# Kernel tuning notes

Measured on AMD Instinct MI355X. Metric: run time of the kernel, lower is better.

The kernel has to match this reference:

```python
import jax, jax.numpy as jnp
import numpy as np

D_MODEL = 1024
N_HEADS = 16
D_K = D_MODEL // N_HEADS
ROPE_BASE = 500000.0
RMS_EPS = 1e-10


def _rms_norm(x, w):
    # RMSNorm over last dim (per-head d_k): w * x / sqrt(mean(x^2) + eps)
    rms = jnp.sqrt(jnp.mean(x * x, axis=-1, keepdims=True) + RMS_EPS)
    return w * (x / rms)


def _rotate_half(x):
    x1, x2 = x[..., : x.shape[-1] // 2], x[..., x.shape[-1] // 2:]
    return jnp.concatenate([-x2, x1], axis=-1)


def _rope_cos_sin(seq_len):
    inv_freq = 1.0 / (ROPE_BASE ** (jnp.arange(0, D_K, 2, dtype=jnp.float32) / D_K))
    t = jnp.arange(seq_len, dtype=jnp.float32)
    freqs = jnp.outer(t, inv_freq)                # (S, d_k/2)
    emb = jnp.concatenate([freqs, freqs], axis=-1)  # (S, d_k)
    return jnp.cos(emb), jnp.sin(emb)


def setup_inputs() -> dict:
    key = jax.random.key(0)
    ks = jax.random.split(key, 9)
    B, S, D = 2, 2048, D_MODEL
    scale = 1.0 / np.sqrt(D)
    return {
        "q": jax.random.normal(ks[0], (B, S, D), jnp.float32),
        "k": jax.random.normal(ks[1], (B, S, D), jnp.float32),
        "v": jax.random.normal(ks[2], (B, S, D), jnp.float32),
        "w_q": jax.random.normal(ks[3], (D, D), jnp.float32) * scale,
        "w_k": jax.random.normal(ks[4], (D, D), jnp.float32) * scale,
        "w_v": jax.random.normal(ks[5], (D, D), jnp.float32) * scale,
        "w_o": jax.random.normal(ks[6], (D, D), jnp.float32) * scale,
        "q_norm_w": jnp.ones((D_K,), jnp.float32),
        "k_norm_w": jnp.ones((D_K,), jnp.float32),
    }


def reference(q, k, v, w_q, w_k, w_v, w_o, q_norm_w, k_norm_w):
    B, S, D = q.shape
    H, Dk = N_HEADS, D_K

    # QKV projections (nn.Linear without bias: x @ W.T), split into heads
    query = jnp.einsum("bsd,ed->bse", q, w_q).reshape(B, S, H, Dk).transpose(0, 2, 1, 3)
    key_ = jnp.einsum("bsd,ed->bse", k, w_k).reshape(B, S, H, Dk).transpose(0, 2, 1, 3)
    value = jnp.einsum("bsd,ed->bse", v, w_v).reshape(B, S, H, Dk).transpose(0, 2, 1, 3)

    # QK-norm (per-head RMSNorm)
    query = _rms_norm(query, q_norm_w)
    key_ = _rms_norm(key_, k_norm_w)

    # RoPE, default positions 0..S-1
    cos, sin = _rope_cos_sin(S)          # (S, d_k)
    cos = cos[None, None]                # (1,1,S,d_k)
    sin = sin[None, None]
    query = query * cos + _rotate_half(query) * sin
    key_ = key_ * cos + _rotate_half(key_) * sin

    # Causal scaled dot-product attention
    scale = 1.0 / jnp.sqrt(jnp.asarray(Dk, query.dtype))
    scores = jnp.einsum("bhqd,bhkd->bhqk", query, key_) * scale
    causal = jnp.tril(jnp.ones((S, S), dtype=bool))
    scores = jnp.where(causal, scores, jnp.finfo(scores.dtype).min)
    attn = jax.nn.softmax(scores, axis=-1)
    out = jnp.einsum("bhqk,bhkd->bhqd", attn, value)  # (B,H,S,d_k)

    out = out.transpose(0, 2, 1, 3).reshape(B, S, D)
    return jnp.einsum("bsd,ed->bse", out, w_o)
```

## Files before the change

### kernel.cpp

```cpp
#include <hip/hip_runtime.h>
#include <cstdint>
#include <cstddef>

typedef __bf16 bf16;
typedef __bf16 bf16x4_t __attribute__((ext_vector_type(4)));
typedef __bf16 bf16x8_t __attribute__((ext_vector_type(8)));
typedef float  f32x4_t  __attribute__((ext_vector_type(4)));

#define GLD_LDS16(g, l)                                                              \
  __builtin_amdgcn_global_load_lds((const __attribute__((address_space(1))) void*)(g), \
                                   (__attribute__((address_space(3))) void*)(l), 16, 0, 0)

#define S_WAITCNT_VMCNT(N) asm volatile("s_waitcnt vmcnt(" #N ")" ::: "memory")
#define S_BARRIER() asm volatile("s_barrier" ::: "memory")

__global__ __launch_bounds__(256) void cvt_kernel(
    const float* __restrict__ q, const float* __restrict__ k, const float* __restrict__ v,
    const float* __restrict__ wq, const float* __restrict__ wk, const float* __restrict__ wv,
    const float* __restrict__ wo,
    bf16* __restrict__ qb, bf16* __restrict__ kb, bf16* __restrict__ vb,
    bf16* __restrict__ wqb, bf16* __restrict__ wkb, bf16* __restrict__ wvb,
    bf16* __restrict__ wob)
{
  const float* src; bf16* dst; int n;
  switch (blockIdx.y) {
    case 0: src = q;  dst = qb;  n = 4194304; break;
    case 1: src = k;  dst = kb;  n = 4194304; break;
    case 2: src = v;  dst = vb;  n = 4194304; break;
    case 3: src = wq; dst = wqb; n = 1048576; break;
    case 4: src = wk; dst = wkb; n = 1048576; break;
    case 5: src = wv; dst = wvb; n = 1048576; break;
    default: src = wo; dst = wob; n = 1048576; break;
  }
  const int i = (blockIdx.x * 256 + threadIdx.x) * 4;
  if (i >= n) return;
  const float4 f = *(const float4*)(src + i);
  bf16x4_t o;
  o[0] = (bf16)f.x; o[1] = (bf16)f.y; o[2] = (bf16)f.z; o[3] = (bf16)f.w;
  *(bf16x4_t*)(dst + i) = o;
}

__device__ __forceinline__ void gemm_core(const bf16* __restrict__ A,
                                          const bf16* __restrict__ W,
                                          int m0, int n0, f32x4_t (&acc)[4][4])
{
  const int K = 1024;
  __shared__ bf16 As[3][128 * 32];
  __shared__ bf16 Bs[3][128 * 32];
  const int t = threadIdx.x;
  const int lane = t & 63, w = t >> 6;
  const int l16 = lane & 15, qd = lane >> 4;
  const int wm = (w & 1) * 64, wn = (w >> 1) * 64;

  const int srow = t >> 2;
  const int skey = (srow & 3) ^ ((srow >> 2) & 3);
  const int scol = ((t & 3) ^ skey) * 8;
  const bf16* ag0 = A + (size_t)(m0 + srow) * K + scol;
  const bf16* ag1 = A + (size_t)(m0 + 64 + srow) * K + scol;
  const bf16* wg0 = W + (size_t)(n0 + srow) * K + scol;
  const bf16* wg1 = W + (size_t)(n0 + 64 + srow) * K + scol;
  const int lo0 = (w * 64) * 8;
  const int lo1 = (256 + w * 64) * 8;

  const int sw = (l16 & 3) ^ ((l16 >> 2) & 3);

#define STAGEG(k0_, b_)                         \
  do {                                          \
    GLD_LDS16(ag0 + (k0_), &As[b_][lo0]);       \
    GLD_LDS16(ag1 + (k0_), &As[b_][lo1]);       \
    GLD_LDS16(wg0 + (k0_), &Bs[b_][lo0]);       \
    GLD_LDS16(wg1 + (k0_), &Bs[b_][lo1]);       \
  } while (0)

  STAGEG(0, 0);
  STAGEG(32, 1);

  for (int k0 = 0; k0 < K; k0 += 32) {
    const int it = k0 >> 5;
    const int cb = it - (it / 3) * 3;
    if (k0 + 32 < K) S_WAITCNT_VMCNT(4); else S_WAITCNT_VMCNT(0);
    S_BARRIER();
    if (k0 + 64 < K) {
      const int nb = (it + 2) - ((it + 2) / 3) * 3;
      STAGEG(k0 + 64, nb);
    }
    bf16x8_t af[4], bfg[4];
#pragma unroll
    for (int i = 0; i < 4; ++i)
      af[i] = *(const bf16x8_t*)(&As[cb][(wm + i * 16 + l16) * 32 + (qd ^ sw) * 8]);
#pragma unroll
    for (int j = 0; j < 4; ++j)
      bfg[j] = *(const bf16x8_t*)(&Bs[cb][(wn + j * 16 + l16) * 32 + (qd ^ sw) * 8]);
#pragma unroll
    for (int i = 0; i < 4; ++i)
#pragma unroll
      for (int j = 0; j < 4; ++j)
        acc[i][j] = __builtin_amdgcn_mfma_f32_16x16x32_bf16(af[i], bfg[j], acc[i][j], 0, 0, 0);
  }
#undef STAGEG
}

__global__ __launch_bounds__(256) void gemm_qkv(
    const bf16* __restrict__ qb, const bf16* __restrict__ wqb,
    const bf16* __restrict__ kb, const bf16* __restrict__ wkb,
    const bf16* __restrict__ vb, const bf16* __restrict__ wvb,
    const float* __restrict__ qnw, const float* __restrict__ knw,
    bf16* __restrict__ Qp, bf16* __restrict__ Kp, bf16* __restrict__ Vt)
{
  const int z = blockIdx.z;
  const bf16 *A, *W;
  if (z == 0)      { A = qb; W = wqb; }
  else if (z == 1) { A = kb; W = wkb; }
  else             { A = vb; W = wvb; }

  const int m0 = blockIdx.y * 128, n0 = blockIdx.x * 128;
  f32x4_t acc[4][4] = {};
  gemm_core(A, W, m0, n0, acc);

  const int t = threadIdx.x;
  const int lane = t & 63, w = t >> 6;
  const int l16 = lane & 15, qd = lane >> 4;
  const int wm = (w & 1) * 64;
  const int h = blockIdx.x * 2 + (w >> 1);
  const int b = m0 >> 11;

  if (z == 2) {
#pragma unroll
    for (int i = 0; i < 4; ++i) {
      const int sq = (m0 & 2047) + wm + i * 16 + qd * 4;
      const int pos = (sq & ~31) + 8 * qd + 4 * (i & 1);
#pragma unroll
      for (int j = 0; j < 4; ++j) {
        const int dk = j * 16 + l16;
        bf16x4_t ov;
#pragma unroll
        for (int r = 0; r < 4; ++r) ov[r] = (bf16)acc[i][j][r];
        *(bf16x4_t*)(Vt + ((size_t)((b * 16 + h) * 64 + dk)) * 2048 + pos) = ov;
      }
    }
    return;
  }

  const float* nw = (z == 0) ? qnw : knw;
  const float osc = (z == 0) ? 0.125f * 1.44269504088896f : 1.0f;
  bf16* Out = (z == 0) ? Qp : Kp;

  float nwv[4];
#pragma unroll
  for (int j = 0; j < 4; ++j) nwv[j] = nw[j * 16 + l16];
  float invf[2];
#pragma unroll
  for (int jj = 0; jj < 2; ++jj) {
    const int d = jj * 16 + l16;
    invf[jj] = __builtin_amdgcn_exp2f(-(float)(2 * d) * (18.93156857f / 64.0f)) * 0.15915494309f;
  }

#pragma unroll
  for (int i = 0; i < 4; ++i) {
    const int sbase = (m0 & 2047) + wm + i * 16 + qd * 4;
    float ssq[4];
#pragma unroll
    for (int r = 0; r < 4; ++r) {
      ssq[r] = 0.f;
#pragma unroll
      for (int j = 0; j < 4; ++j) ssq[r] += acc[i][j][r] * acc[i][j][r];
    }
#pragma unroll
    for (int off = 1; off < 16; off <<= 1)
#pragma unroll
      for (int r = 0; r < 4; ++r) ssq[r] += __shfl_xor(ssq[r], off);

    float xn[4][4];
#pragma unroll
    for (int r = 0; r < 4; ++r) {
      const float inv = 1.0f / sqrtf(ssq[r] * (1.0f / 64.0f) + 1e-10f);
#pragma unroll
      for (int j = 0; j < 4; ++j) xn[j][r] = acc[i][j][r] * inv * nwv[j];
    }
#pragma unroll
    for (int jj = 0; jj < 2; ++jj) {
      const int d = jj * 16 + l16;
#pragma unroll
      for (int r = 0; r < 4; ++r) {
        const int s = sbase + r;
        float rev = (float)s * invf[jj];
        rev = rev - floorf(rev);
        const float cv = __builtin_amdgcn_cosf(rev);
        const float sv = __builtin_amdgcn_sinf(rev);
        const float o1 = (xn[jj][r] * cv - xn[jj + 2][r] * sv) * osc;
        const float o2 = (xn[jj + 2][r] * cv + xn[jj][r] * sv) * osc;
        bf16* base = Out + ((size_t)(b * 16 + h) * 2048 + s) * 64;
        base[d] = (bf16)o1;
        base[d + 32] = (bf16)o2;
      }
    }
  }
}

__global__ __launch_bounds__(256) void gemm_out_k(
    const bf16* __restrict__ Ob, const bf16* __restrict__ wob, float* __restrict__ out)
{
  const int N = 1024;
  const int m0 = blockIdx.y * 128, n0 = blockIdx.x * 128;
  f32x4_t acc[4][4] = {};
  gemm_core(Ob, wob, m0, n0, acc);

  const int t = threadIdx.x;
  const int lane = t & 63, w = t >> 6;
  const int l16 = lane & 15, qd = lane >> 4;
  const int wm = (w & 1) * 64, wn = (w >> 1) * 64;
#pragma unroll
  for (int i = 0; i < 4; ++i) {
    const int row = m0 + wm + i * 16 + qd * 4;
#pragma unroll
    for (int j = 0; j < 4; ++j) {
      const int col = n0 + wn + j * 16 + l16;
#pragma unroll
      for (int r = 0; r < 4; ++r)
        out[(size_t)(row + r) * N + col] = acc[i][j][r];
    }
  }
}

__global__ __launch_bounds__(512) void flash_attn(
    const bf16* __restrict__ Qp, const bf16* __restrict__ Kp,
    const bf16* __restrict__ Vt, bf16* __restrict__ O)
{
  const int S = 2048;
  const int qt = 15 - blockIdx.x;
  const int bh = blockIdx.y;
  const int t = threadIdx.x;
  const int lane = t & 63, w = t >> 6;
  const int l16 = lane & 15, qd = lane >> 4;

  __shared__ bf16 Ks[3][64 * 64];
  __shared__ bf16 Vs[3][64 * 64];

  const int qrow = qt * 128 + w * 16 + l16;
  const bf16* qbase = Qp + ((size_t)bh * S + qrow) * 64 + qd * 8;
  const bf16x8_t qf0 = *(const bf16x8_t*)qbase;
  const bf16x8_t qf1 = *(const bf16x8_t*)(qbase + 32);

  f32x4_t o_acc[4] = {};
  float l_i = 0.f;

  const int srow = t >> 3;
  const int scol = ((t & 7) ^ (srow & 7)) * 8;
  const bf16* kg = Kp + ((size_t)bh * S + srow) * 64 + scol;
  const bf16* vg = Vt + ((size_t)(bh * 64 + srow)) * S + scol;
  const int lo = w * 512;

  const int sw = l16 & 7;

#define STAGE(kt_, b_)                                 \
  do {                                                 \
    GLD_LDS16(kg + (size_t)(kt_) * 4096, &Ks[b_][lo]); \
    GLD_LDS16(vg + (kt_) * 64, &Vs[b_][lo]);           \
  } while (0)

  const int ktmax = 2 * qt + 1;
  STAGE(0, 0);
  STAGE(1, 1);

  for (int kt = 0; kt <= ktmax; ++kt) {
    const int cb = kt - (kt / 3) * 3;
    if (kt < ktmax) S_WAITCNT_VMCNT(2); else S_WAITCNT_VMCNT(0);
    S_BARRIER();
    if (kt + 2 <= ktmax) {
      const int nb = (kt + 2) - ((kt + 2) / 3) * 3;
      STAGE(kt + 2, nb);
    }

    if (kt == ktmax && w < 4) continue;

    f32x4_t sf[4];
#pragma unroll
    for (int nt = 0; nt < 4; ++nt) {
      sf[nt][0] = -12.f; sf[nt][1] = -12.f; sf[nt][2] = -12.f; sf[nt][3] = -12.f;
      const bf16x8_t kf0 = *(const bf16x8_t*)(&Ks[cb][(nt * 16 + l16) * 64 + ((0 + qd) ^ sw) * 8]);
      const bf16x8_t kf1 = *(const bf16x8_t*)(&Ks[cb][(nt * 16 + l16) * 64 + ((4 + qd) ^ sw) * 8]);
      sf[nt] = __builtin_amdgcn_mfma_f32_16x16x32_bf16(kf0, qf0, sf[nt], 0, 0, 0);
      sf[nt] = __builtin_amdgcn_mfma_f32_16x16x32_bf16(kf1, qf1, sf[nt], 0, 0, 0);
    }

    if (kt >= ktmax - 1) {
      const int kofs = (kt - 2 * qt) * 64;
      const int q_local = w * 16 + l16;
#pragma unroll
      for (int nt = 0; nt < 4; ++nt)
#pragma unroll
        for (int r = 0; r < 4; ++r)
          if (kofs + nt * 16 + qd * 4 + r > q_local) sf[nt][r] = -100.f;
    }

    bf16x4_t pb[4];
#pragma unroll
    for (int nt = 0; nt < 4; ++nt)
#pragma unroll
      for (int r = 0; r < 4; ++r) {
        const float p = __builtin_amdgcn_exp2f(sf[nt][r]);
        l_i += p;
        pb[nt][r] = (bf16)p;
      }

#pragma unroll
    for (int nt2 = 0; nt2 < 2; ++nt2) {
      bf16x8_t pf;
#pragma unroll
      for (int r = 0; r < 4; ++r) { pf[r] = pb[2 * nt2][r]; pf[4 + r] = pb[2 * nt2 + 1][r]; }
#pragma unroll
      for (int dt = 0; dt < 4; ++dt) {
        const int row = dt * 16 + l16;
        const bf16x8_t vf =
            *(const bf16x8_t*)(&Vs[cb][row * 64 + ((4 * nt2 + qd) ^ sw) * 8]);
        o_acc[dt] = __builtin_amdgcn_mfma_f32_16x16x32_bf16(vf, pf, o_acc[dt], 0, 0, 0);
      }
    }
  }
#undef STAGE

  l_i += __shfl_xor(l_i, 16);
  l_i += __shfl_xor(l_i, 32);

  const int b = bh >> 4, h = bh & 15;
  const float inv_l = 1.0f / l_i;
  const int qg = qt * 128 + w * 16 + l16;
#pragma unroll
  for (int dt = 0; dt < 4; ++dt) {
    bf16x4_t ov;
#pragma unroll
    for (int r = 0; r < 4; ++r) ov[r] = (bf16)(o_acc[dt][r] * inv_l);
    *(bf16x4_t*)(O + ((size_t)(b * S + qg)) * 1024 + h * 64 + dt * 16 + qd * 4) = ov;
  }
}

extern "C" void kernel_launch(void* const* d_in, const int* in_sizes, int n_in,
                              void* d_out, int out_size, void* d_ws, size_t ws_size,
                              hipStream_t stream)
{
  const float* q   = (const float*)d_in[0];
  const float* k   = (const float*)d_in[1];
  const float* v   = (const float*)d_in[2];
  const float* wq  = (const float*)d_in[3];
  const float* wk  = (const float*)d_in[4];
  const float* wv  = (const float*)d_in[5];
  const float* wo  = (const float*)d_in[6];
  const float* qnw = (const float*)d_in[7];
  const float* knw = (const float*)d_in[8];

  char* ws = (char*)d_ws;
  const size_t MB = 1u << 20;
  bf16* qb  = (bf16*)(ws + 0 * MB);
  bf16* kb  = (bf16*)(ws + 8 * MB);
  bf16* vb  = (bf16*)(ws + 16 * MB);
  bf16* wqb = (bf16*)(ws + 24 * MB);
  bf16* wkb = (bf16*)(ws + 26 * MB);
  bf16* wvb = (bf16*)(ws + 28 * MB);
  bf16* wob = (bf16*)(ws + 30 * MB);
  bf16* Qp  = (bf16*)(ws + 32 * MB);
  bf16* Kp  = (bf16*)(ws + 40 * MB);
  bf16* Vtr = (bf16*)(ws + 48 * MB);
  bf16* Oattn = qb;

  cvt_kernel<<<dim3(4096, 7), 256, 0, stream>>>(q, k, v, wq, wk, wv, wo,
                                                qb, kb, vb, wqb, wkb, wvb, wob);
  gemm_qkv<<<dim3(8, 32, 3), 256, 0, stream>>>(qb, wqb, kb, wkb, vb, wvb,
                                               qnw, knw, Qp, Kp, Vtr);
  flash_attn<<<dim3(16, 32), 512, 0, stream>>>(Qp, Kp, Vtr, Oattn);
  gemm_out_k<<<dim3(8, 32), 256, 0, stream>>>(Oattn, wob, (float*)d_out);
}
```

Before: 226.9 us.

## Repack GEMM LDS tile swizzle and stage epilogues through LDS for vector stores

Changes the shared-memory layout of the GEMM staging tiles to a new XOR swizzle that packs two rows per 64-element line, aimed at cutting LDS bank conflicts on both the global_load_lds writes and the MFMA fragment reads. The QKV and output-projection epilogues now write results into a per-wave padded LDS scratch region and then issue 16-byte vector global stores per row. This replaces scattered 2-byte bf16 and 4-byte float stores. It adds a block-wide barrier and extra LDS traffic in the epilogue, and it reuses the staging buffer for scratch.

```diff
diff --git a/kernel.cpp b/kernel.cpp
--- a/kernel.cpp
+++ b/kernel.cpp
@@ -42,34 +42,38 @@
 
 __device__ __forceinline__ void gemm_core(const bf16* __restrict__ A,
                                           const bf16* __restrict__ W,
-                                          int m0, int n0, f32x4_t (&acc)[4][4])
+                                          int m0, int n0, bf16* smem,
+                                          f32x4_t (&acc)[4][4])
 {
   const int K = 1024;
-  __shared__ bf16 As[3][128 * 32];
-  __shared__ bf16 Bs[3][128 * 32];
+  bf16* As = smem;
+  bf16* Bs = smem + 12288;
   const int t = threadIdx.x;
   const int lane = t & 63, w = t >> 6;
   const int l16 = lane & 15, qd = lane >> 4;
   const int wm = (w & 1) * 64, wn = (w >> 1) * 64;
 
-  const int srow = t >> 2;
-  const int skey = (srow & 3) ^ ((srow >> 2) & 3);
-  const int scol = ((t & 3) ^ skey) * 8;
-  const bf16* ag0 = A + (size_t)(m0 + srow) * K + scol;
-  const bf16* ag1 = A + (size_t)(m0 + 64 + srow) * K + scol;
-  const bf16* wg0 = W + (size_t)(n0 + srow) * K + scol;
-  const bf16* wg1 = W + (size_t)(n0 + 64 + srow) * K + scol;
+  const int p8 = t >> 3;
+  const int vslot = (t & 7) ^ (p8 & 7);
+  const int srow = 2 * p8 + (vslot >> 2);
+  const int scc = vslot & 3;
+  const bf16* ag0 = A + (size_t)(m0 + srow) * K + scc * 8;
+  const bf16* ag1 = A + (size_t)(m0 + 64 + srow) * K + scc * 8;
+  const bf16* wg0 = W + (size_t)(n0 + srow) * K + scc * 8;
+  const bf16* wg1 = W + (size_t)(n0 + 64 + srow) * K + scc * 8;
   const int lo0 = (w * 64) * 8;
   const int lo1 = (256 + w * 64) * 8;
 
-  const int sw = (l16 & 3) ^ ((l16 >> 2) & 3);
-
-#define STAGEG(k0_, b_)                         \
-  do {                                          \
-    GLD_LDS16(ag0 + (k0_), &As[b_][lo0]);       \
-    GLD_LDS16(ag1 + (k0_), &As[b_][lo1]);       \
-    GLD_LDS16(wg0 + (k0_), &Bs[b_][lo0]);       \
-    GLD_LDS16(wg1 + (k0_), &Bs[b_][lo1]);       \
+  const int rslot = (((l16 & 1) * 4 + qd) ^ ((l16 >> 1) & 7)) * 8;
+  const int abase = (wm >> 6) * 2048 + (l16 >> 1) * 64 + rslot;
+  const int bbase = (wn >> 6) * 2048 + (l16 >> 1) * 64 + rslot;
+
+#define STAGEG(k0_, b_)                                  \
+  do {                                                   \
+    GLD_LDS16(ag0 + (k0_), &As[(b_) * 4096 + lo0]);      \
+    GLD_LDS16(ag1 + (k0_), &As[(b_) * 4096 + lo1]);      \
+    GLD_LDS16(wg0 + (k0_), &Bs[(b_) * 4096 + lo0]);      \
+    GLD_LDS16(wg1 + (k0_), &Bs[(b_) * 4096 + lo1]);      \
   } while (0)
 
   STAGEG(0, 0);
@@ -87,10 +91,10 @@
     bf16x8_t af[4], bfg[4];
 #pragma unroll
     for (int i = 0; i < 4; ++i)
-      af[i] = *(const bf16x8_t*)(&As[cb][(wm + i * 16 + l16) * 32 + (qd ^ sw) * 8]);
+      af[i] = *(const bf16x8_t*)(&As[cb * 4096 + abase + i * 512]);
 #pragma unroll
     for (int j = 0; j < 4; ++j)
-      bfg[j] = *(const bf16x8_t*)(&Bs[cb][(wn + j * 16 + l16) * 32 + (qd ^ sw) * 8]);
+      bfg[j] = *(const bf16x8_t*)(&Bs[cb * 4096 + bbase + j * 512]);
 #pragma unroll
     for (int i = 0; i < 4; ++i)
 #pragma unroll
@@ -107,6 +111,7 @@
     const float* __restrict__ qnw, const float* __restrict__ knw,
     bf16* __restrict__ Qp, bf16* __restrict__ Kp, bf16* __restrict__ Vt)
 {
+  __shared__ bf16 smem[24576];
   const int z = blockIdx.z;
   const bf16 *A, *W;
   if (z == 0)      { A = qb; W = wqb; }
@@ -115,7 +120,7 @@
 
   const int m0 = blockIdx.y * 128, n0 = blockIdx.x * 128;
   f32x4_t acc[4][4] = {};
-  gemm_core(A, W, m0, n0, acc);
+  gemm_core(A, W, m0, n0, smem, acc);
 
   const int t = threadIdx.x;
   const int lane = t & 63, w = t >> 6;
@@ -155,6 +160,9 @@
     invf[jj] = __builtin_amdgcn_exp2f(-(float)(2 * d) * (18.93156857f / 64.0f)) * 0.15915494309f;
   }
 
+  __syncthreads();
+  bf16* ep = smem + w * 1152;
+
 #pragma unroll
   for (int i = 0; i < 4; ++i) {
     const int sbase = (m0 & 2047) + wm + i * 16 + qd * 4;
@@ -179,7 +187,6 @@
     }
 #pragma unroll
     for (int jj = 0; jj < 2; ++jj) {
-      const int d = jj * 16 + l16;
 #pragma unroll
       for (int r = 0; r < 4; ++r) {
         const int s = sbase + r;
@@ -189,35 +196,49 @@
         const float sv = __builtin_amdgcn_sinf(rev);
         const float o1 = (xn[jj][r] * cv - xn[jj + 2][r] * sv) * osc;
         const float o2 = (xn[jj + 2][r] * cv + xn[jj][r] * sv) * osc;
-        bf16* base = Out + ((size_t)(b * 16 + h) * 2048 + s) * 64;
-        base[d] = (bf16)o1;
-        base[d + 32] = (bf16)o2;
+        const int prow = qd * 4 + r;
+        ep[prow * 72 + jj * 16 + l16] = (bf16)o1;
+        ep[prow * 72 + 32 + jj * 16 + l16] = (bf16)o2;
       }
     }
+    const int sg = (m0 & 2047) + wm + i * 16 + l16;
+    const bf16x8_t t0 = *(const bf16x8_t*)(ep + l16 * 72 + qd * 16);
+    const bf16x8_t t1 = *(const bf16x8_t*)(ep + l16 * 72 + qd * 16 + 8);
+    bf16* gb = Out + ((size_t)(b * 16 + h) * 2048 + sg) * 64 + qd * 16;
+    *(bf16x8_t*)(gb) = t0;
+    *(bf16x8_t*)(gb + 8) = t1;
   }
 }
 
 __global__ __launch_bounds__(256) void gemm_out_k(
     const bf16* __restrict__ Ob, const bf16* __restrict__ wob, float* __restrict__ out)
 {
+  __shared__ bf16 smem[24576];
   const int N = 1024;
   const int m0 = blockIdx.y * 128, n0 = blockIdx.x * 128;
   f32x4_t acc[4][4] = {};
-  gemm_core(Ob, wob, m0, n0, acc);
+  gemm_core(Ob, wob, m0, n0, smem, acc);
 
   const int t = threadIdx.x;
   const int lane = t & 63, w = t >> 6;
   const int l16 = lane & 15, qd = lane >> 4;
   const int wm = (w & 1) * 64, wn = (w >> 1) * 64;
+
+  __syncthreads();
+  float* epf = (float*)smem + w * 1088;
+
 #pragma unroll
   for (int i = 0; i < 4; ++i) {
-    const int row = m0 + wm + i * 16 + qd * 4;
-#pragma unroll
-    for (int j = 0; j < 4; ++j) {
-      const int col = n0 + wn + j * 16 + l16;
+#pragma unroll
+    for (int j = 0; j < 4; ++j)
 #pragma unroll
       for (int r = 0; r < 4; ++r)
-        out[(size_t)(row + r) * N + col] = acc[i][j][r];
+        epf[(qd * 4 + r) * 68 + j * 16 + l16] = acc[i][j][r];
+    const int row = m0 + wm + i * 16 + l16;
+#pragma unroll
+    for (int c = 0; c < 4; ++c) {
+      const f32x4_t vv = *(const f32x4_t*)(epf + l16 * 68 + qd * 16 + c * 4);
+      *(f32x4_t*)(out + (size_t)row * N + n0 + wn + qd * 16 + c * 4) = vv;
     }
   }
 }
```

Result: faster. 214.4 us (-5.5%).
